# Performance work log

Hardware: AMD Instinct MI355X
Metric: run time of the kernel (lower is better)

## Reference

```python
import jax, jax.numpy as jnp
import numpy as np

EXP_EMBD = 1024
EXP_Q_H = 8
EXP_HEAD_DIM = 256
EXP_KV_H = 1
EXP_KV_DIM = EXP_KV_H * EXP_HEAD_DIM  # 256
EXP_FFN = 4096
B, L, LC = 8, 512, 2048


def setup_inputs() -> dict:
    key = jax.random.key(0)
    ks = jax.random.split(key, 12)
    def w(k, shape):
        fan_in = shape[-1]
        return jax.random.normal(k, shape, jnp.float32) * (fan_in ** -0.5)
    return {
        "x": jax.random.normal(ks[0], (B, L, EXP_EMBD), jnp.float32),
        "text_k": jax.random.normal(ks[1], (B, LC, EXP_KV_DIM), jnp.float32),
        "text_v": jax.random.normal(ks[2], (B, LC, EXP_KV_DIM), jnp.float32),
        "ln1_w": jnp.ones((EXP_EMBD,), jnp.float32),
        "ln2_w": jnp.ones((EXP_EMBD,), jnp.float32),
        "Wq": w(ks[3], (EXP_Q_H * EXP_HEAD_DIM, EXP_EMBD)),
        "Wk": w(ks[4], (EXP_KV_DIM, EXP_KV_DIM)),
        "Wv": w(ks[5], (EXP_KV_DIM, EXP_KV_DIM)),
        "Wo": w(ks[6], (EXP_EMBD, EXP_Q_H * EXP_HEAD_DIM)),
        "Wg": w(ks[7], (EXP_FFN, EXP_EMBD)),
        "Wu": w(ks[8], (EXP_FFN, EXP_EMBD)),
        "Wd": w(ks[9], (EXP_EMBD, EXP_FFN)),
    }


def _rmsnorm(x, w):
    # torch.nn.RMSNorm with eps=None -> eps = finfo(dtype).eps
    eps = jnp.asarray(jnp.finfo(jnp.float32).eps, x.dtype)
    return x * jax.lax.rsqrt(jnp.mean(x * x, axis=-1, keepdims=True) + eps) * w


def _rope(x):
    # x: [B, L, H, D]
    b, l, h, d = x.shape
    d2 = d // 2
    ts = 10000.0 ** (2.0 / d * jnp.arange(d2, dtype=jnp.float32))  # [d2]
    rad = jnp.arange(l, dtype=jnp.float32)[:, None] / ts[None, :]  # [L, d2]
    s = jnp.sin(rad)[None, :, None, :]
    c = jnp.cos(rad)[None, :, None, :]
    x1, x2 = x[..., :d2], x[..., d2:]
    return jnp.concatenate([x1 * c - x2 * s, x2 * c + x1 * s], axis=-1)


def reference(x, text_k, text_v, ln1_w, ln2_w, Wq, Wk, Wv, Wo, Wg, Wu, Wd):
    b, l, _ = x.shape
    lc = text_k.shape[1]
    residual = x
    h = _rmsnorm(x, ln1_w)
    q = _rope((h @ Wq.T).reshape(b, l, EXP_Q_H, EXP_HEAD_DIM))          # [B,L,QH,D]
    k = (text_k @ Wk.T).reshape(b, lc, EXP_KV_H, EXP_HEAD_DIM)          # [B,Lc,KVH,D]
    v = (text_v @ Wv.T).reshape(b, lc, EXP_KV_H, EXP_HEAD_DIM)
    kv_map = (jnp.arange(EXP_Q_H) * EXP_KV_H) // EXP_Q_H                # GQA head map
    kh = jnp.take(k, kv_map, axis=2)                                    # [B,Lc,QH,D]
    vh = jnp.take(v, kv_map, axis=2)
    scale = 1.0 / np.sqrt(EXP_HEAD_DIM).astype(np.float32)
    scores = jnp.einsum('blhd,bchd->bhlc', q, kh) * scale               # [B,QH,L,Lc]
    attn = jax.nn.softmax(scores, axis=-1)
    ctx = jnp.einsum('bhlc,bchd->blhd', attn, vh).reshape(b, l, -1)
    x = ctx @ Wo.T + residual
    residual = x
    h = _rmsnorm(x, ln2_w)
    return (jax.nn.silu(h @ Wg.T) * (h @ Wu.T)) @ Wd.T + residual
```

## Files before the change

kernel.cpp:

```cpp
#include <hip/hip_runtime.h>

typedef __attribute__((ext_vector_type(4))) float f32x4;
typedef __attribute__((ext_vector_type(8))) short s16x8;
typedef __attribute__((ext_vector_type(4))) unsigned short u16x4;

#define B_    8
#define L_    512
#define LC_   2048
#define EMBD  1024

__device__ __forceinline__ float b2f(unsigned short u) {
  unsigned int i = ((unsigned int)u) << 16;
  float f; __builtin_memcpy(&f, &i, 4); return f;
}
__device__ __forceinline__ unsigned short f2b(float f) {
  unsigned int i; __builtin_memcpy(&i, &f, 4);
  unsigned int r = i + 0x7FFFu + ((i >> 16) & 1u);
  return (unsigned short)(r >> 16);
}

#define GLL16(g, l)                                                         \
  __builtin_amdgcn_global_load_lds(                                         \
      (__attribute__((address_space(1))) void*)(g),                         \
      (__attribute__((address_space(3))) void*)(l), 16, 0, 0)

#define VMCNT6() asm volatile("s_waitcnt vmcnt(6)" ::: "memory")
#define VMCNT0() asm volatile("s_waitcnt vmcnt(0)" ::: "memory")
#define LGKM0()  asm volatile("s_waitcnt lgkmcnt(0)" ::: "memory")

__global__ __launch_bounds__(256) void convert9(
    const float* s0, const float* s1, const float* s2, const float* s3,
    const float* s4, const float* s5, const float* s6, const float* s7,
    const float* s8,
    unsigned short* d0, unsigned short* d1, unsigned short* d2,
    unsigned short* d3, unsigned short* d4, unsigned short* d5,
    unsigned short* d6, unsigned short* d7, unsigned short* d8) {
  int bk = blockIdx.x;
  const float* s; unsigned short* d; int base;
  if      (bk <  2048) { s = s0; d = d0; base = 0; }
  else if (bk <  2112) { s = s1; d = d1; base = 2048; }
  else if (bk <  2176) { s = s2; d = d2; base = 2112; }
  else if (bk <  4224) { s = s3; d = d3; base = 2176; }
  else if (bk <  8320) { s = s4; d = d4; base = 4224; }
  else if (bk < 12416) { s = s5; d = d5; base = 8320; }
  else if (bk < 16512) { s = s6; d = d6; base = 12416; }
  else if (bk < 20608) { s = s7; d = d7; base = 16512; }
  else                 { s = s8; d = d8; base = 20608; }
  int i = (bk - base) * 256 + threadIdx.x;
  float4 v = ((const float4*)s)[i];
  u16x4 o = { f2b(v.x), f2b(v.y), f2b(v.z), f2b(v.w) };
  ((u16x4*)d)[i] = o;
}

__global__ __launch_bounds__(256) void rmsnorm_kernel(
    const float* __restrict__ x, const float* __restrict__ w,
    unsigned short* __restrict__ out) {
  int row = blockIdx.x;
  int tid = threadIdx.x;
  float4 v = ((const float4*)(x + (size_t)row * EMBD))[tid];
  float ss = v.x*v.x + v.y*v.y + v.z*v.z + v.w*v.w;
#pragma unroll
  for (int o = 1; o < 64; o <<= 1) ss += __shfl_xor(ss, o);
  __shared__ float red[4];
  if ((tid & 63) == 0) red[tid >> 6] = ss;
  __syncthreads();
  float tot = red[0] + red[1] + red[2] + red[3];
  float rs = rsqrtf(tot * (1.0f / EMBD) + 1.1920928955078125e-07f);
  float4 wv = ((const float4*)w)[tid];
  u16x4 o = { f2b(v.x*rs*wv.x), f2b(v.y*rs*wv.y), f2b(v.z*rs*wv.z), f2b(v.w*rs*wv.w) };
  ((u16x4*)(out + (size_t)row * EMBD))[tid] = o;
}

__global__ __launch_bounds__(256) void rope_kernel(unsigned short* __restrict__ q) {
  int idx = blockIdx.x * 256 + threadIdx.x;
  int i   = idx & 127;
  int h   = (idx >> 7) & 7;
  int row = idx >> 10;
  int l   = row & (L_ - 1);
  size_t base = (size_t)row * 2048 + h * 256 + i;
  float x1 = b2f(q[base]);
  float x2 = b2f(q[base + 128]);
  float ts  = powf(10000.0f, (float)i * (2.0f / 256.0f));
  float rad = (float)l / ts;
  float s, c;
  sincosf(rad, &s, &c);
  q[base]       = f2b(x1 * c - x2 * s);
  q[base + 128] = f2b(x2 * c + x1 * s);
}

template <int ADD_RES, int OUT_BF16>
__global__ __launch_bounds__(256, 2) void gemm_nt(
    const unsigned short* __restrict__ A, const unsigned short* __restrict__ Bw,
    const float* __restrict__ Res, void* __restrict__ C, int M, int N, int K) {
  __shared__ unsigned short As[128 * 64];
  __shared__ unsigned short Bs[128 * 64];
  const int tid = threadIdx.x;
  const int lane = tid & 63, wid = tid >> 6;
  const int l15 = lane & 15, l4 = lane >> 4;
  const int wr = wid >> 1, wc = wid & 1;
  const int m0 = blockIdx.y * 128, n0 = blockIdx.x * 128;

  const f32x4 fz = {0.f, 0.f, 0.f, 0.f};
  f32x4 acc[4][4];
#pragma unroll
  for (int i = 0; i < 4; ++i)
#pragma unroll
    for (int j = 0; j < 4; ++j) acc[i][j] = fz;

  for (int k0 = 0; k0 < K; k0 += 64) {
    __syncthreads();
#pragma unroll
    for (int i = 0; i < 4; ++i) {
      int Li = i * 4096 + tid * 16;
      int row = Li >> 7;
      int kb = (Li & 127) ^ ((row & 7) << 4);
      GLL16((const char*)(A + (size_t)(m0 + row) * K + k0) + kb, (char*)As + Li);
      GLL16((const char*)(Bw + (size_t)(n0 + row) * K + k0) + kb, (char*)Bs + Li);
    }
    __syncthreads();
#pragma unroll
    for (int kk = 0; kk < 2; ++kk) {
      s16x8 af[4], bfr[4];
#pragma unroll
      for (int mi = 0; mi < 4; ++mi) {
        int row = wr * 64 + mi * 16 + l15;
        int kb = (kk * 64 + l4 * 16) ^ ((row & 7) << 4);
        af[mi] = *(const s16x8*)((const char*)As + row * 128 + kb);
      }
#pragma unroll
      for (int ni = 0; ni < 4; ++ni) {
        int row = wc * 64 + ni * 16 + l15;
        int kb = (kk * 64 + l4 * 16) ^ ((row & 7) << 4);
        bfr[ni] = *(const s16x8*)((const char*)Bs + row * 128 + kb);
      }
#pragma unroll
      for (int mi = 0; mi < 4; ++mi)
#pragma unroll
        for (int ni = 0; ni < 4; ++ni)
          acc[mi][ni] = __builtin_amdgcn_mfma_f32_16x16x32_bf16(
              af[mi], bfr[ni], acc[mi][ni], 0, 0, 0);
    }
  }
#pragma unroll
  for (int mi = 0; mi < 4; ++mi) {
#pragma unroll
    for (int r = 0; r < 4; ++r) {
      int grow = m0 + wr * 64 + mi * 16 + l4 * 4 + r;
      size_t base = (size_t)grow * N + n0 + wc * 64 + l15;
#pragma unroll
      for (int ni = 0; ni < 4; ++ni) {
        float v = acc[mi][ni][r];
        size_t idx = base + ni * 16;
        if (ADD_RES) v += Res[idx];
        if (OUT_BF16) ((unsigned short*)C)[idx] = f2b(v);
        else          ((float*)C)[idx] = v;
      }
    }
  }
}

template <int ADD_RES, int OUT_BF16>
__global__ __launch_bounds__(256, 2) void gemm_nt64(
    const unsigned short* __restrict__ A, const unsigned short* __restrict__ Bw,
    const float* __restrict__ Res, void* __restrict__ C, int M, int N, int K) {
  __shared__ unsigned short As[64 * 64];
  __shared__ unsigned short Bs[128 * 64];
  const int tid = threadIdx.x;
  const int lane = tid & 63, wid = tid >> 6;
  const int l15 = lane & 15, l4 = lane >> 4;
  const int wr = wid >> 1, wc = wid & 1;
  const int m0 = blockIdx.y * 64, n0 = blockIdx.x * 128;

  const f32x4 fz = {0.f, 0.f, 0.f, 0.f};
  f32x4 acc[2][4];
#pragma unroll
  for (int i = 0; i < 2; ++i)
#pragma unroll
    for (int j = 0; j < 4; ++j) acc[i][j] = fz;

  for (int k0 = 0; k0 < K; k0 += 64) {
    __syncthreads();
#pragma unroll
    for (int i = 0; i < 2; ++i) {
      int Li = i * 4096 + tid * 16;
      int row = Li >> 7;
      int kb = (Li & 127) ^ ((row & 7) << 4);
      GLL16((const char*)(A + (size_t)(m0 + row) * K + k0) + kb, (char*)As + Li);
    }
#pragma unroll
    for (int i = 0; i < 4; ++i) {
      int Li = i * 4096 + tid * 16;
      int row = Li >> 7;
      int kb = (Li & 127) ^ ((row & 7) << 4);
      GLL16((const char*)(Bw + (size_t)(n0 + row) * K + k0) + kb, (char*)Bs + Li);
    }
    __syncthreads();
#pragma unroll
    for (int kk = 0; kk < 2; ++kk) {
      s16x8 af[2], bfr[4];
#pragma unroll
      for (int mi = 0; mi < 2; ++mi) {
        int row = wr * 32 + mi * 16 + l15;
        int kb = (kk * 64 + l4 * 16) ^ ((row & 7) << 4);
        af[mi] = *(const s16x8*)((const char*)As + row * 128 + kb);
      }
#pragma unroll
      for (int ni = 0; ni < 4; ++ni) {
        int row = wc * 64 + ni * 16 + l15;
        int kb = (kk * 64 + l4 * 16) ^ ((row & 7) << 4);
        bfr[ni] = *(const s16x8*)((const char*)Bs + row * 128 + kb);
      }
#pragma unroll
      for (int mi = 0; mi < 2; ++mi)
#pragma unroll
        for (int ni = 0; ni < 4; ++ni)
          acc[mi][ni] = __builtin_amdgcn_mfma_f32_16x16x32_bf16(
              af[mi], bfr[ni], acc[mi][ni], 0, 0, 0);
    }
  }
#pragma unroll
  for (int mi = 0; mi < 2; ++mi) {
#pragma unroll
    for (int r = 0; r < 4; ++r) {
      int grow = m0 + wr * 32 + mi * 16 + l4 * 4 + r;
      size_t base = (size_t)grow * N + n0 + wc * 64 + l15;
#pragma unroll
      for (int ni = 0; ni < 4; ++ni) {
        float v = acc[mi][ni][r];
        size_t idx = base + ni * 16;
        if (ADD_RES) v += Res[idx];
        if (OUT_BF16) ((unsigned short*)C)[idx] = f2b(v);
        else          ((float*)C)[idx] = v;
      }
    }
  }
}

template <int SWIGLU>
__global__ __launch_bounds__(512, 2) void gemm256(
    const unsigned short* __restrict__ A, const unsigned short* __restrict__ Bw,
    const unsigned short* __restrict__ G, unsigned short* __restrict__ C,
    int M, int N, int K) {
  extern __shared__ char smem[];
  const int tid = threadIdx.x;
  const int lane = tid & 63;
  const int wid = tid >> 6;
  const int wr = wid >> 2, wc = wid & 3;
  const int l15 = lane & 15, g = lane >> 4;
  int flat = blockIdx.y * 16 + blockIdx.x;
  flat = (flat & 7) * 32 + (flat >> 3);
  const int m0 = (flat >> 4) * 256, n0 = (flat & 15) * 256;
  const int T = K >> 6;
  const int swz = (l15 & 7) << 4;

  auto stage = [&](int t, int mat, int half) {
    char* dst = smem + mat * 65536 + (t & 1) * 32768 + half * 16384;
    const unsigned short* src = (mat ? Bw + (size_t)(n0 + half * 128) * K
                                     : A + (size_t)(m0 + half * 128) * K) + t * 64;
#pragma unroll
    for (int i = 0; i < 2; ++i) {
      int Li = i * 8192 + tid * 16;
      int row = Li >> 7;
      int kb = (Li & 127) ^ ((row & 7) << 4);
      GLL16((const char*)(src + (size_t)row * K) + kb, dst + Li);
    }
  };

  const f32x4 fz = {0.f, 0.f, 0.f, 0.f};
  f32x4 acc[2][2][4][2];
#pragma unroll
  for (int ms = 0; ms < 2; ++ms)
#pragma unroll
    for (int ns = 0; ns < 2; ++ns)
#pragma unroll
      for (int mi = 0; mi < 4; ++mi)
#pragma unroll
        for (int ni = 0; ni < 2; ++ni) acc[ms][ns][mi][ni] = fz;

  stage(0, 1, 0); stage(0, 1, 1); stage(0, 0, 0); stage(0, 0, 1);
  stage(1, 1, 0); stage(1, 1, 1); stage(1, 0, 0);
  VMCNT6();
  __builtin_amdgcn_s_barrier();

  for (int t = 0; t < T; ++t) {
    char* Ab = smem + (t & 1) * 32768 + wr * 16384;
    char* Bb = smem + 65536 + (t & 1) * 32768 + (wc >> 1) * 16384;
    const int bn = (wc & 1) * 64;
    s16x8 a[4][2], b0[2][2], b1[2][2];

#pragma unroll
    for (int mi = 0; mi < 4; ++mi) {
      int row = mi * 16 + l15;
#pragma unroll
      for (int kk = 0; kk < 2; ++kk)
        a[mi][kk] = *(const s16x8*)(Ab + row * 128 + ((kk * 64 + g * 16) ^ swz));
    }
#pragma unroll
    for (int ni = 0; ni < 2; ++ni) {
      int r0 = (bn + ni * 16 + l15) * 128;
      int r1 = (bn + 32 + ni * 16 + l15) * 128;
#pragma unroll
      for (int kk = 0; kk < 2; ++kk) {
        int ko = (kk * 64 + g * 16) ^ swz;
        b0[ni][kk] = *(const s16x8*)(Bb + r0 + ko);
        b1[ni][kk] = *(const s16x8*)(Bb + r1 + ko);
      }
    }
    if (t + 1 < T) stage(t + 1, 0, 1);
    __builtin_amdgcn_s_barrier();
    LGKM0();
    __builtin_amdgcn_sched_barrier(0);
    __builtin_amdgcn_s_setprio(1);
#pragma unroll
    for (int mi = 0; mi < 4; ++mi)
#pragma unroll
      for (int ni = 0; ni < 2; ++ni)
#pragma unroll
        for (int kk = 0; kk < 2; ++kk)
          acc[0][0][mi][ni] = __builtin_amdgcn_mfma_f32_16x16x32_bf16(
              a[mi][kk], b0[ni][kk], acc[0][0][mi][ni], 0, 0, 0);
    __builtin_amdgcn_s_setprio(0);
    __builtin_amdgcn_s_barrier();

    if (t + 2 < T) stage(t + 2, 1, 0);
    __builtin_amdgcn_s_barrier();
    __builtin_amdgcn_s_setprio(1);
#pragma unroll
    for (int mi = 0; mi < 4; ++mi)
#pragma unroll
      for (int ni = 0; ni < 2; ++ni)
#pragma unroll
        for (int kk = 0; kk < 2; ++kk)
          acc[0][1][mi][ni] = __builtin_amdgcn_mfma_f32_16x16x32_bf16(
              a[mi][kk], b1[ni][kk], acc[0][1][mi][ni], 0, 0, 0);
    __builtin_amdgcn_s_setprio(0);
    __builtin_amdgcn_s_barrier();

#pragma unroll
    for (int mi = 0; mi < 4; ++mi) {
      int row = 64 + mi * 16 + l15;
#pragma unroll
      for (int kk = 0; kk < 2; ++kk)
        a[mi][kk] = *(const s16x8*)(Ab + row * 128 + ((kk * 64 + g * 16) ^ swz));
    }
    if (t + 2 < T) stage(t + 2, 1, 1);
    __builtin_amdgcn_s_barrier();
    LGKM0();
    __builtin_amdgcn_sched_barrier(0);
    __builtin_amdgcn_s_setprio(1);
#pragma unroll
    for (int mi = 0; mi < 4; ++mi)
#pragma unroll
      for (int ni = 0; ni < 2; ++ni)
#pragma unroll
        for (int kk = 0; kk < 2; ++kk)
          acc[1][0][mi][ni] = __builtin_amdgcn_mfma_f32_16x16x32_bf16(
              a[mi][kk], b0[ni][kk], acc[1][0][mi][ni], 0, 0, 0);
    __builtin_amdgcn_s_setprio(0);
    __builtin_amdgcn_s_barrier();

    if (t + 2 < T) { stage(t + 2, 0, 0); VMCNT6(); }
    else           { VMCNT0(); }
    __builtin_amdgcn_s_barrier();
    __builtin_amdgcn_s_setprio(1);
#pragma unroll
    for (int mi = 0; mi < 4; ++mi)
#pragma unroll
      for (int ni = 0; ni < 2; ++ni)
#pragma unroll
        for (int kk = 0; kk < 2; ++kk)
          acc[1][1][mi][ni] = __builtin_amdgcn_mfma_f32_16x16x32_bf16(
              a[mi][kk], b1[ni][kk], acc[1][1][mi][ni], 0, 0, 0);
    __builtin_amdgcn_s_setprio(0);
    __builtin_amdgcn_s_barrier();
  }

#pragma unroll
  for (int ms = 0; ms < 2; ++ms)
#pragma unroll
    for (int mi = 0; mi < 4; ++mi)
#pragma unroll
      for (int r = 0; r < 4; ++r) {
        int grow = m0 + wr * 128 + ms * 64 + mi * 16 + g * 4 + r;
        size_t base = (size_t)grow * N + n0 + wc * 64;
#pragma unroll
        for (int ns = 0; ns < 2; ++ns)
#pragma unroll
          for (int ni = 0; ni < 2; ++ni) {
            size_t idx = base + ns * 32 + ni * 16 + l15;
            float v = acc[ms][ns][mi][ni][r];
            if (SWIGLU) {
              float gf = b2f(G[idx]);
              v *= gf / (1.0f + __expf(-gf));
            }
            C[idx] = f2b(v);
          }
      }
}

#define SWZV(d) (((((d) & 7) ^ (((d) >> 3) & 7))) << 4)

__global__ __launch_bounds__(512, 2) void attn_kernel(
    const unsigned short* __restrict__ Q,
    const unsigned short* __restrict__ Kc,
    const unsigned short* __restrict__ Vc,
    unsigned short* __restrict__ Op0, unsigned short* __restrict__ Op1,
    float2* __restrict__ Ml0, float2* __restrict__ Ml1) {
  extern __shared__ char ats[];
  const int tid = threadIdx.x;
  const int lane = tid & 63, wid = tid >> 6;
  const int l15 = lane & 15, g = lane >> 4;
  const int qt = blockIdx.x, h = blockIdx.y;
  const int b = blockIdx.z >> 1, half = blockIdx.z & 1;

  const size_t qrow = (size_t)(b * L_ + qt * 128 + wid * 16 + l15);
  const unsigned short* qp = Q + qrow * 2048 + h * 256;
  s16x8 qf[8];
#pragma unroll
  for (int kc = 0; kc < 8; ++kc) qf[kc] = *(const s16x8*)(qp + kc * 32 + g * 8);

  const f32x4 fz = {0.f, 0.f, 0.f, 0.f};
  f32x4 oacc[16];
#pragma unroll
  for (int i = 0; i < 16; ++i) oacc[i] = fz;
  float m_run = -__builtin_inff(), l_run = 0.f;

  const unsigned short* Kb = Kc + (size_t)b * LC_ * 256;
  const unsigned short* Vb = Vc + (size_t)b * LC_ * 256;

  auto stageK = [&](int kt, char* dstK) {
#pragma unroll
    for (int i = 0; i < 4; ++i) {
      int Li = i * 8192 + tid * 16;
      int row = Li >> 9;
      int kb = (Li & 511) ^ ((row & 7) << 4);
      GLL16((const char*)(Kb + (size_t)(kt * 64 + row) * 256) + kb, dstK + Li);
    }
  };
  s16x8 vr[2][2];
  auto loadV = [&](int kt) {
#pragma unroll
    for (int p = 0; p < 2; ++p) {
      int id = p * 512 + tid;
      int dgrp = id & 31, kvp = id >> 5;
      const unsigned short* v0p = Vb + (size_t)(kt * 64 + kvp * 2) * 256 + dgrp * 8;
      vr[p][0] = *(const s16x8*)v0p;
      vr[p][1] = *(const s16x8*)(v0p + 256);
    }
  };
  auto writeV = [&](char* dstV) {
#pragma unroll
    for (int p = 0; p < 2; ++p) {
      int id = p * 512 + tid;
      int dgrp = id & 31, kvp = id >> 5;
      int d0 = dgrp * 8, kv0 = kvp * 2;
#pragma unroll
      for (int j = 0; j < 8; ++j) {
        int d = d0 + j;
        unsigned int val = (unsigned int)(unsigned short)vr[p][0][j] |
                           ((unsigned int)(unsigned short)vr[p][1][j] << 16);
        *(unsigned int*)(dstV + d * 128 + ((kv0 * 2) ^ SWZV(d))) = val;
      }
    }
  };

  const int kt0 = half * 16, ktE = kt0 + 16;
  stageK(kt0, ats);
  loadV(kt0);
  VMCNT0();
  writeV(ats + 65536);
  __syncthreads();

  for (int kt = kt0; kt < ktE; ++kt) {
    const int cur = (kt - kt0) & 1, nxt = cur ^ 1;
    char* KsB = ats + cur * 32768;
    char* VtB = ats + 65536 + cur * 32768;
    const bool more = (kt + 1 < ktE);
    if (more) { stageK(kt + 1, ats + nxt * 32768); loadV(kt + 1); }

    f32x4 sacc[4];
#pragma unroll
    for (int mi = 0; mi < 4; ++mi) sacc[mi] = fz;
#pragma unroll
    for (int mi = 0; mi < 4; ++mi) {
      int row = mi * 16 + l15;
      int swz = (row & 7) << 4;
#pragma unroll
      for (int kc = 0; kc < 8; ++kc) {
        s16x8 kf = *(const s16x8*)(KsB + row * 512 + ((kc * 64 + g * 16) ^ swz));
        sacc[mi] = __builtin_amdgcn_mfma_f32_16x16x32_bf16(kf, qf[kc], sacc[mi], 0, 0, 0);
      }
    }
    float sv[4][4];
    float mt = -__builtin_inff();
#pragma unroll
    for (int mi = 0; mi < 4; ++mi)
#pragma unroll
      for (int r = 0; r < 4; ++r) {
        float t = sacc[mi][r] * 0.0625f;
        sv[mi][r] = t;
        mt = fmaxf(mt, t);
      }
    mt = fmaxf(mt, __shfl_xor(mt, 16));
    mt = fmaxf(mt, __shfl_xor(mt, 32));
    if (!__all(mt <= m_run + 8.0f)) {
      float mnew = fmaxf(m_run, mt);
      float alpha = __expf(m_run - mnew);
      float af4[4];
#pragma unroll
      for (int r = 0; r < 4; ++r) af4[r] = __shfl(alpha, g * 4 + r);
#pragma unroll
      for (int nd = 0; nd < 16; ++nd)
#pragma unroll
        for (int r = 0; r < 4; ++r) oacc[nd][r] *= af4[r];
      l_run *= alpha;
      m_run = mnew;
    }
    float rs = 0.f;
#pragma unroll
    for (int mi = 0; mi < 4; ++mi)
#pragma unroll
      for (int r = 0; r < 4; ++r) {
        float p = __expf(sv[mi][r] - m_run);
        sv[mi][r] = p;
        rs += p;
      }
    rs += __shfl_xor(rs, 16);
    rs += __shfl_xor(rs, 32);
    l_run += rs;
    unsigned int pk[4][2];
#pragma unroll
    for (int ni = 0; ni < 4; ++ni) {
      pk[ni][0] = (unsigned int)f2b(sv[ni][0]) | ((unsigned int)f2b(sv[ni][1]) << 16);
      pk[ni][1] = (unsigned int)f2b(sv[ni][2]) | ((unsigned int)f2b(sv[ni][3]) << 16);
    }
    int cbase = (g & 1) << 3;
#pragma unroll
    for (int tt = 0; tt < 2; ++tt) {
      unsigned int w[4];
#pragma unroll
      for (int jj = 0; jj < 4; ++jj) {
        int c = cbase + (jj << 1);
        int src = ((c >> 2) << 4) + l15;
        unsigned int ra = __shfl(pk[2 * tt][jj & 1], src);
        unsigned int rb = __shfl(pk[2 * tt + 1][jj & 1], src);
        w[jj] = (g < 2) ? ra : rb;
      }
      union { unsigned int u[4]; s16x8 v; } cvt;
      cvt.u[0] = w[0]; cvt.u[1] = w[1]; cvt.u[2] = w[2]; cvt.u[3] = w[3];
      s16x8 ap = cvt.v;
#pragma unroll
      for (int nd = 0; nd < 16; ++nd) {
        int d = nd * 16 + l15;
        s16x8 vf = *(const s16x8*)(VtB + d * 128 + ((tt * 64 + g * 16) ^ SWZV(d)));
        oacc[nd] = __builtin_amdgcn_mfma_f32_16x16x32_bf16(ap, vf, oacc[nd], 0, 0, 0);
      }
    }

    if (more) { VMCNT0(); writeV(ats + 65536 + nxt * 32768); }
    __syncthreads();
  }
  unsigned short* Op = half ? Op1 : Op0;
  float2* Ml = half ? Ml1 : Ml0;
  float lf[4];
#pragma unroll
  for (int r = 0; r < 4; ++r) lf[r] = 1.0f / __shfl(l_run, g * 4 + r);
  const size_t orow0 = (size_t)(b * L_ + qt * 128 + wid * 16);
#pragma unroll
  for (int r = 0; r < 4; ++r) {
    size_t base = (orow0 + g * 4 + r) * 2048 + h * 256 + l15;
#pragma unroll
    for (int nd = 0; nd < 16; ++nd)
      Op[base + nd * 16] = f2b(oacc[nd][r] * lf[r]);
  }
  if (g == 0) Ml[(orow0 + l15) * 8 + h] = make_float2(m_run, l_run);
}

__global__ __launch_bounds__(256) void attn_merge(
    const unsigned short* __restrict__ p0, const unsigned short* __restrict__ p1,
    const float2* __restrict__ ml0, const float2* __restrict__ ml1,
    unsigned short* __restrict__ ctx) {
  int i = blockIdx.x * 256 + threadIdx.x;
  int rowh = i >> 5;
  int dch = i & 31;
  float2 a = ml0[rowh], c = ml1[rowh];
  float M = fmaxf(a.x, c.x);
  float w0 = a.y * __expf(a.x - M), w1 = c.y * __expf(c.x - M);
  float inv = 1.0f / (w0 + w1);
  w0 *= inv; w1 *= inv;
  int row = rowh >> 3, h = rowh & 7;
  size_t off = (size_t)row * 2048 + h * 256 + dch * 8;
  s16x8 v0 = *(const s16x8*)(p0 + off);
  s16x8 v1 = *(const s16x8*)(p1 + off);
  s16x8 o;
#pragma unroll
  for (int j = 0; j < 8; ++j)
    o[j] = (short)f2b(w0 * b2f((unsigned short)v0[j]) + w1 * b2f((unsigned short)v1[j]));
  *(s16x8*)(ctx + off) = o;
}

extern "C" void kernel_launch(void* const* d_in, const int* in_sizes, int n_in,
                              void* d_out, int out_size, void* d_ws, size_t ws_size,
                              hipStream_t stream) {
  const float* x   = (const float*)d_in[0];
  const float* tk  = (const float*)d_in[1];
  const float* tv  = (const float*)d_in[2];
  const float* ln1 = (const float*)d_in[3];
  const float* ln2 = (const float*)d_in[4];
  const float* Wq  = (const float*)d_in[5];
  const float* Wk  = (const float*)d_in[6];
  const float* Wv  = (const float*)d_in[7];
  const float* Wo  = (const float*)d_in[8];
  const float* Wg  = (const float*)d_in[9];
  const float* Wu  = (const float*)d_in[10];
  const float* Wd  = (const float*)d_in[11];
  float* out = (float*)d_out;
  char* ws = (char*)d_ws;

  (void)hipFuncSetAttribute((const void*)gemm256<0>,
                            hipFuncAttributeMaxDynamicSharedMemorySize, 131072);
  (void)hipFuncSetAttribute((const void*)gemm256<1>,
                            hipFuncAttributeMaxDynamicSharedMemorySize, 131072);
  (void)hipFuncSetAttribute((const void*)attn_kernel,
                            hipFuncAttributeMaxDynamicSharedMemorySize, 131072);

  unsigned short* tk_bf  = (unsigned short*)(ws + 0);
  unsigned short* tv_bf  = (unsigned short*)(ws + 8388608);
  unsigned short* k_bf   = (unsigned short*)(ws + 16777216);
  unsigned short* v_bf   = (unsigned short*)(ws + 25165824);
  unsigned short* g_bf   = (unsigned short*)(ws + 0);
  unsigned short* op0    = (unsigned short*)(ws + 0);
  unsigned short* q_bf   = (unsigned short*)(ws + 33554432);
  unsigned short* ctx_bf = (unsigned short*)(ws + 50331648);
  unsigned short* u_bf   = (unsigned short*)(ws + 33554432);
  unsigned short* wq_bf  = (unsigned short*)(ws + 67108864);
  unsigned short* wk_bf  = (unsigned short*)(ws + 71303168);
  unsigned short* wv_bf  = (unsigned short*)(ws + 71434240);
  unsigned short* wo_bf  = (unsigned short*)(ws + 71565312);
  unsigned short* wg_bf  = (unsigned short*)(ws + 75759616);
  unsigned short* wu_bf  = (unsigned short*)(ws + 84148224);
  unsigned short* wd_bf  = (unsigned short*)(ws + 92536832);
  unsigned short* h_bf   = (unsigned short*)(ws + 100925440);
  float2*         ml0    = (float2*)(ws + 100925440);
  float2*         ml1    = (float2*)(ws + 100925440 + 262144);
  float*          x2     = (float*)(ws + 109314048);
  unsigned short* op1    = (unsigned short*)(ws + 109314048);

  dim3 blk(256);
  convert9<<<dim3(24704), blk, 0, stream>>>(
      Wq, Wk, Wv, Wo, Wg, Wu, Wd, tk, tv,
      wq_bf, wk_bf, wv_bf, wo_bf, wg_bf, wu_bf, wd_bf, tk_bf, tv_bf);

  rmsnorm_kernel<<<dim3(4096), blk, 0, stream>>>(x, ln1, h_bf);
  gemm_nt<0, 1><<<dim3(16, 32), blk, 0, stream>>>(h_bf, wq_bf, nullptr, q_bf, 4096, 2048, 1024);
  rope_kernel<<<dim3(16384), blk, 0, stream>>>(q_bf);
  gemm_nt64<0, 1><<<dim3(2, 256), blk, 0, stream>>>(tk_bf, wk_bf, nullptr, k_bf, 16384, 256, 256);
  gemm_nt64<0, 1><<<dim3(2, 256), blk, 0, stream>>>(tv_bf, wv_bf, nullptr, v_bf, 16384, 256, 256);
  attn_kernel<<<dim3(4, 8, 16), dim3(512), 131072, stream>>>(q_bf, k_bf, v_bf, op0, op1, ml0, ml1);
  attn_merge<<<dim3(4096), blk, 0, stream>>>(op0, op1, ml0, ml1, ctx_bf);
  gemm_nt64<1, 0><<<dim3(8, 64), blk, 0, stream>>>(ctx_bf, wo_bf, x, x2, 4096, 1024, 2048);
  rmsnorm_kernel<<<dim3(4096), blk, 0, stream>>>(x2, ln2, h_bf);
  gemm256<0><<<dim3(16, 16), dim3(512), 131072, stream>>>(h_bf, wg_bf, nullptr, g_bf, 4096, 4096, 1024);
  gemm256<1><<<dim3(16, 16), dim3(512), 131072, stream>>>(h_bf, wu_bf, g_bf, g_bf, 4096, 4096, 1024);
  gemm_nt64<1, 0><<<dim3(8, 64), blk, 0, stream>>>(g_bf, wd_bf, x2, out, 4096, 1024, 4096);
}
```

Measured before the change: 400.4 us.

## Rewrite attention with 32x32 MFMA, 256-row Q tiles, single-buffered LDS

The attention kernel moves from 16x16x32 to 32x32x16 bf16 MFMA, with each wave owning 32 query rows, so each block covers 256 queries and the grid halves. The double-buffered K/V prefetch pipeline is replaced by a single static 64KB LDS buffer with synchronous staging between two barriers. Larger tiles give more reuse of each K/V tile and fewer blocks re-reading K/V. The cost is lost load/compute overlap, more registers per thread (16 Q fragments, 128 accumulator floats), and only 256 blocks, which may underfill the GPU.

New measurement: 500.4 us. +25.0%, slower.

```diff
diff --git a/kernel.cpp b/kernel.cpp
--- a/kernel.cpp
+++ b/kernel.cpp
@@ -1,6 +1,7 @@
 #include <hip/hip_runtime.h>
 
 typedef __attribute__((ext_vector_type(4))) float f32x4;
+typedef __attribute__((ext_vector_type(16))) float f32x16;
 typedef __attribute__((ext_vector_type(8))) short s16x8;
 typedef __attribute__((ext_vector_type(4))) unsigned short u16x4;
 
@@ -406,174 +407,149 @@
     const unsigned short* __restrict__ Vc,
     unsigned short* __restrict__ Op0, unsigned short* __restrict__ Op1,
     float2* __restrict__ Ml0, float2* __restrict__ Ml1) {
-  extern __shared__ char ats[];
+  __shared__ unsigned short Ks[64 * 256];
+  __shared__ unsigned short Vt[256 * 64];
   const int tid = threadIdx.x;
   const int lane = tid & 63, wid = tid >> 6;
-  const int l15 = lane & 15, g = lane >> 4;
+  const int l31 = lane & 31, hi = lane >> 5;
   const int qt = blockIdx.x, h = blockIdx.y;
   const int b = blockIdx.z >> 1, half = blockIdx.z & 1;
 
-  const size_t qrow = (size_t)(b * L_ + qt * 128 + wid * 16 + l15);
-  const unsigned short* qp = Q + qrow * 2048 + h * 256;
-  s16x8 qf[8];
-#pragma unroll
-  for (int kc = 0; kc < 8; ++kc) qf[kc] = *(const s16x8*)(qp + kc * 32 + g * 8);
-
-  const f32x4 fz = {0.f, 0.f, 0.f, 0.f};
-  f32x4 oacc[16];
-#pragma unroll
-  for (int i = 0; i < 16; ++i) oacc[i] = fz;
+  const size_t qrow = (size_t)(b * L_ + qt * 256 + wid * 32 + l31);
+  const unsigned short* qp = Q + qrow * 2048 + h * 256 + hi * 8;
+  s16x8 qf[16];
+#pragma unroll
+  for (int kc = 0; kc < 16; ++kc) qf[kc] = *(const s16x8*)(qp + kc * 16);
+
+  f32x16 oacc[8];
+#pragma unroll
+  for (int dg = 0; dg < 8; ++dg)
+#pragma unroll
+    for (int r = 0; r < 16; ++r) oacc[dg][r] = 0.f;
   float m_run = -__builtin_inff(), l_run = 0.f;
 
   const unsigned short* Kb = Kc + (size_t)b * LC_ * 256;
   const unsigned short* Vb = Vc + (size_t)b * LC_ * 256;
 
-  auto stageK = [&](int kt, char* dstK) {
+  const int kt0 = half * 16, ktE = kt0 + 16;
+  for (int kt = kt0; kt < ktE; ++kt) {
+    __syncthreads();
 #pragma unroll
     for (int i = 0; i < 4; ++i) {
       int Li = i * 8192 + tid * 16;
       int row = Li >> 9;
       int kb = (Li & 511) ^ ((row & 7) << 4);
-      GLL16((const char*)(Kb + (size_t)(kt * 64 + row) * 256) + kb, dstK + Li);
-    }
-  };
-  s16x8 vr[2][2];
-  auto loadV = [&](int kt) {
-#pragma unroll
-    for (int p = 0; p < 2; ++p) {
-      int id = p * 512 + tid;
-      int dgrp = id & 31, kvp = id >> 5;
-      const unsigned short* v0p = Vb + (size_t)(kt * 64 + kvp * 2) * 256 + dgrp * 8;
-      vr[p][0] = *(const s16x8*)v0p;
-      vr[p][1] = *(const s16x8*)(v0p + 256);
-    }
-  };
-  auto writeV = [&](char* dstV) {
+      GLL16((const char*)(Kb + (size_t)(kt * 64 + row) * 256) + kb, (char*)Ks + Li);
+    }
 #pragma unroll
     for (int p = 0; p < 2; ++p) {
       int id = p * 512 + tid;
       int dgrp = id & 31, kvp = id >> 5;
       int d0 = dgrp * 8, kv0 = kvp * 2;
+      const unsigned short* v0p = Vb + (size_t)(kt * 64 + kv0) * 256 + d0;
+      s16x8 r0 = *(const s16x8*)v0p;
+      s16x8 r1 = *(const s16x8*)(v0p + 256);
 #pragma unroll
       for (int j = 0; j < 8; ++j) {
         int d = d0 + j;
-        unsigned int val = (unsigned int)(unsigned short)vr[p][0][j] |
-                           ((unsigned int)(unsigned short)vr[p][1][j] << 16);
-        *(unsigned int*)(dstV + d * 128 + ((kv0 * 2) ^ SWZV(d))) = val;
-      }
-    }
-  };
-
-  const int kt0 = half * 16, ktE = kt0 + 16;
-  stageK(kt0, ats);
-  loadV(kt0);
-  VMCNT0();
-  writeV(ats + 65536);
-  __syncthreads();
-
-  for (int kt = kt0; kt < ktE; ++kt) {
-    const int cur = (kt - kt0) & 1, nxt = cur ^ 1;
-    char* KsB = ats + cur * 32768;
-    char* VtB = ats + 65536 + cur * 32768;
-    const bool more = (kt + 1 < ktE);
-    if (more) { stageK(kt + 1, ats + nxt * 32768); loadV(kt + 1); }
-
-    f32x4 sacc[4];
-#pragma unroll
-    for (int mi = 0; mi < 4; ++mi) sacc[mi] = fz;
-#pragma unroll
-    for (int mi = 0; mi < 4; ++mi) {
-      int row = mi * 16 + l15;
-      int swz = (row & 7) << 4;
-#pragma unroll
-      for (int kc = 0; kc < 8; ++kc) {
-        s16x8 kf = *(const s16x8*)(KsB + row * 512 + ((kc * 64 + g * 16) ^ swz));
-        sacc[mi] = __builtin_amdgcn_mfma_f32_16x16x32_bf16(kf, qf[kc], sacc[mi], 0, 0, 0);
-      }
-    }
-    float sv[4][4];
+        unsigned int val = (unsigned int)(unsigned short)r0[j] |
+                           ((unsigned int)(unsigned short)r1[j] << 16);
+        *(unsigned int*)((char*)Vt + d * 128 + ((kv0 * 2) ^ SWZV(d))) = val;
+      }
+    }
+    __syncthreads();
+
+    f32x16 s0, s1;
+#pragma unroll
+    for (int r = 0; r < 16; ++r) { s0[r] = 0.f; s1[r] = 0.f; }
+#pragma unroll
+    for (int kc = 0; kc < 16; ++kc) {
+      int ko = (kc * 32 + hi * 16);
+      int row0 = l31, row1 = 32 + l31;
+      s16x8 kf0 = *(const s16x8*)((const char*)Ks + row0 * 512 + (ko ^ ((row0 & 7) << 4)));
+      s16x8 kf1 = *(const s16x8*)((const char*)Ks + row1 * 512 + (ko ^ ((row1 & 7) << 4)));
+      s0 = __builtin_amdgcn_mfma_f32_32x32x16_bf16(kf0, qf[kc], s0, 0, 0, 0);
+      s1 = __builtin_amdgcn_mfma_f32_32x32x16_bf16(kf1, qf[kc], s1, 0, 0, 0);
+    }
+
+    float sv[2][16];
     float mt = -__builtin_inff();
 #pragma unroll
-    for (int mi = 0; mi < 4; ++mi)
-#pragma unroll
-      for (int r = 0; r < 4; ++r) {
-        float t = sacc[mi][r] * 0.0625f;
-        sv[mi][r] = t;
-        mt = fmaxf(mt, t);
-      }
-    mt = fmaxf(mt, __shfl_xor(mt, 16));
+    for (int r = 0; r < 16; ++r) {
+      sv[0][r] = s0[r] * 0.0625f;
+      sv[1][r] = s1[r] * 0.0625f;
+      mt = fmaxf(mt, fmaxf(sv[0][r], sv[1][r]));
+    }
     mt = fmaxf(mt, __shfl_xor(mt, 32));
     if (!__all(mt <= m_run + 8.0f)) {
       float mnew = fmaxf(m_run, mt);
       float alpha = __expf(m_run - mnew);
-      float af4[4];
-#pragma unroll
-      for (int r = 0; r < 4; ++r) af4[r] = __shfl(alpha, g * 4 + r);
-#pragma unroll
-      for (int nd = 0; nd < 16; ++nd)
-#pragma unroll
-        for (int r = 0; r < 4; ++r) oacc[nd][r] *= af4[r];
+#pragma unroll
+      for (int r = 0; r < 16; ++r) {
+        float af = __shfl(alpha, (r & 3) + 8 * (r >> 2) + 4 * hi);
+#pragma unroll
+        for (int dg = 0; dg < 8; ++dg) oacc[dg][r] *= af;
+      }
       l_run *= alpha;
       m_run = mnew;
     }
     float rs = 0.f;
 #pragma unroll
-    for (int mi = 0; mi < 4; ++mi)
-#pragma unroll
-      for (int r = 0; r < 4; ++r) {
+    for (int mi = 0; mi < 2; ++mi)
+#pragma unroll
+      for (int r = 0; r < 16; ++r) {
         float p = __expf(sv[mi][r] - m_run);
         sv[mi][r] = p;
         rs += p;
       }
-    rs += __shfl_xor(rs, 16);
     rs += __shfl_xor(rs, 32);
     l_run += rs;
-    unsigned int pk[4][2];
-#pragma unroll
-    for (int ni = 0; ni < 4; ++ni) {
-      pk[ni][0] = (unsigned int)f2b(sv[ni][0]) | ((unsigned int)f2b(sv[ni][1]) << 16);
-      pk[ni][1] = (unsigned int)f2b(sv[ni][2]) | ((unsigned int)f2b(sv[ni][3]) << 16);
-    }
-    int cbase = (g & 1) << 3;
-#pragma unroll
-    for (int tt = 0; tt < 2; ++tt) {
-      unsigned int w[4];
-#pragma unroll
-      for (int jj = 0; jj < 4; ++jj) {
-        int c = cbase + (jj << 1);
-        int src = ((c >> 2) << 4) + l15;
-        unsigned int ra = __shfl(pk[2 * tt][jj & 1], src);
-        unsigned int rb = __shfl(pk[2 * tt + 1][jj & 1], src);
-        w[jj] = (g < 2) ? ra : rb;
-      }
-      union { unsigned int u[4]; s16x8 v; } cvt;
-      cvt.u[0] = w[0]; cvt.u[1] = w[1]; cvt.u[2] = w[2]; cvt.u[3] = w[3];
-      s16x8 ap = cvt.v;
-#pragma unroll
-      for (int nd = 0; nd < 16; ++nd) {
-        int d = nd * 16 + l15;
-        s16x8 vf = *(const s16x8*)(VtB + d * 128 + ((tt * 64 + g * 16) ^ SWZV(d)));
-        oacc[nd] = __builtin_amdgcn_mfma_f32_16x16x32_bf16(ap, vf, oacc[nd], 0, 0, 0);
-      }
-    }
-
-    if (more) { VMCNT0(); writeV(ats + 65536 + nxt * 32768); }
-    __syncthreads();
+
+    unsigned int pkf[16];
+#pragma unroll
+    for (int mi = 0; mi < 2; ++mi)
+#pragma unroll
+      for (int rr = 0; rr < 8; ++rr)
+        pkf[mi * 8 + rr] = (unsigned int)f2b(sv[mi][2 * rr]) |
+                           ((unsigned int)f2b(sv[mi][2 * rr + 1]) << 16);
+
+#pragma unroll
+    for (int ks = 0; ks < 4; ++ks) {
+      unsigned int keep0 = hi ? pkf[4 * ks + 2] : pkf[4 * ks];
+      unsigned int keep1 = hi ? pkf[4 * ks + 3] : pkf[4 * ks + 1];
+      unsigned int send0 = hi ? pkf[4 * ks]     : pkf[4 * ks + 2];
+      unsigned int send1 = hi ? pkf[4 * ks + 1] : pkf[4 * ks + 3];
+      unsigned int recv0 = __shfl_xor(send0, 32);
+      unsigned int recv1 = __shfl_xor(send1, 32);
+      union { unsigned int u[4]; s16x8 v; } pf;
+      pf.u[0] = hi ? recv0 : keep0;
+      pf.u[1] = hi ? recv1 : keep1;
+      pf.u[2] = hi ? keep0 : recv0;
+      pf.u[3] = hi ? keep1 : recv1;
+      int ko = ks * 32 + hi * 16;
+#pragma unroll
+      for (int dg = 0; dg < 8; ++dg) {
+        int d = dg * 32 + l31;
+        s16x8 vf = *(const s16x8*)((const char*)Vt + d * 128 + (ko ^ SWZV(d)));
+        oacc[dg] = __builtin_amdgcn_mfma_f32_32x32x16_bf16(pf.v, vf, oacc[dg], 0, 0, 0);
+      }
+    }
   }
+
   unsigned short* Op = half ? Op1 : Op0;
   float2* Ml = half ? Ml1 : Ml0;
-  float lf[4];
-#pragma unroll
-  for (int r = 0; r < 4; ++r) lf[r] = 1.0f / __shfl(l_run, g * 4 + r);
-  const size_t orow0 = (size_t)(b * L_ + qt * 128 + wid * 16);
-#pragma unroll
-  for (int r = 0; r < 4; ++r) {
-    size_t base = (orow0 + g * 4 + r) * 2048 + h * 256 + l15;
-#pragma unroll
-    for (int nd = 0; nd < 16; ++nd)
-      Op[base + nd * 16] = f2b(oacc[nd][r] * lf[r]);
+  float inv = 1.0f / l_run;
+  const size_t orow0 = (size_t)(b * L_ + qt * 256 + wid * 32);
+#pragma unroll
+  for (int r = 0; r < 16; ++r) {
+    int qr = (r & 3) + 8 * (r >> 2) + 4 * hi;
+    float lfr = __shfl(inv, qr);
+    size_t base = (orow0 + qr) * 2048 + h * 256 + l31;
+#pragma unroll
+    for (int dg = 0; dg < 8; ++dg)
+      Op[base + dg * 32] = f2b(oacc[dg][r] * lfr);
   }
-  if (g == 0) Ml[(orow0 + l15) * 8 + h] = make_float2(m_run, l_run);
+  if (lane < 32) Ml[(orow0 + lane) * 8 + h] = make_float2(m_run, l_run);
 }
 
 __global__ __launch_bounds__(256) void attn_merge(
@@ -620,8 +596,6 @@
   (void)hipFuncSetAttribute((const void*)gemm256<0>,
                             hipFuncAttributeMaxDynamicSharedMemorySize, 131072);
   (void)hipFuncSetAttribute((const void*)gemm256<1>,
-                            hipFuncAttributeMaxDynamicSharedMemorySize, 131072);
-  (void)hipFuncSetAttribute((const void*)attn_kernel,
                             hipFuncAttributeMaxDynamicSharedMemorySize, 131072);
 
   unsigned short* tk_bf  = (unsigned short*)(ws + 0);
@@ -656,7 +630,7 @@
   rope_kernel<<<dim3(16384), blk, 0, stream>>>(q_bf);
   gemm_nt64<0, 1><<<dim3(2, 256), blk, 0, stream>>>(tk_bf, wk_bf, nullptr, k_bf, 16384, 256, 256);
   gemm_nt64<0, 1><<<dim3(2, 256), blk, 0, stream>>>(tv_bf, wv_bf, nullptr, v_bf, 16384, 256, 256);
-  attn_kernel<<<dim3(4, 8, 16), dim3(512), 131072, stream>>>(q_bf, k_bf, v_bf, op0, op1, ml0, ml1);
+  attn_kernel<<<dim3(2, 8, 16), dim3(512), 0, stream>>>(q_bf, k_bf, v_bf, op0, op1, ml0, ml1);
   attn_merge<<<dim3(4096), blk, 0, stream>>>(op0, op1, ml0, ml1, ctx_bf);
   gemm_nt64<1, 0><<<dim3(8, 64), blk, 0, stream>>>(ctx_bf, wo_bf, x, x2, 4096, 1024, 2048);
   rmsnorm_kernel<<<dim3(4096), blk, 0, stream>>>(x2, ln2, h_bf);
```
